# Kernel optimization log

Hardware: AMD Instinct MI355X
Metric: run time of the kernel (lower is better)

## Reference

```python
import jax, jax.numpy as jnp
import numpy as np

N = 50000          # number of keys
T = 12             # time_steps
Q = 3              # n_quantiles
H = 64             # hidden_channels
K = 32             # max children per key (keybom width)
NUM_LEVELS = 4     # hierarchy levels 0..3


def setup_inputs() -> dict:
    key = jax.random.key(0)
    k1, k2, k3, k4, k5, k6, k7 = jax.random.split(key, 7)
    gnn_embedding = jax.random.normal(k1, (N * T, H), dtype=jnp.float32)
    proj_w = jax.random.normal(k2, (H, Q), dtype=jnp.float32) * 0.1
    proj_b = jax.random.normal(k3, (Q,), dtype=jnp.float32) * 0.1
    # positive scaler (divided by later)
    scaler = jax.random.uniform(k4, (N, T), dtype=jnp.float32) + 0.5
    keybom = jax.random.randint(k5, (N, K), 0, N, dtype=jnp.int64)
    pad = jax.random.uniform(k6, (N, K)) < 0.3
    keybom = jnp.where(pad, jnp.int64(-1), keybom)
    key_level_index = jax.random.randint(k7, (N, 1), 0, NUM_LEVELS, dtype=jnp.int64)
    return {
        "gnn_embedding": gnn_embedding,
        "proj_w": proj_w,
        "proj_b": proj_b,
        "scaler": scaler,
        "keybom": keybom,
        "key_level_index": key_level_index,
        "num_levels": NUM_LEVELS,
    }


def reference(gnn_embedding, proj_w, proj_b, scaler, keybom, key_level_index, num_levels):
    n = scaler.shape[0]
    t = scaler.shape[1]
    q = proj_w.shape[1]
    # projection_layer + reshape (-1, time_steps, n_quantiles)
    out = (gnn_embedding @ proj_w + proj_b).reshape(n, t, q)  # [N,T,Q]
    # append dummy zero row (index n) used for -1 padding in keybom
    out = jnp.concatenate([out, jnp.zeros((1, t, q), out.dtype)], axis=0)      # [N+1,T,Q]
    sc = jnp.concatenate(
        [scaler[:, :, None], jnp.ones((1, t, 1), scaler.dtype)], axis=0
    )                                                                          # [N+1,T,1]
    kb = jnp.where(keybom < 0, n, keybom)  # -1 -> dummy row
    lvl = key_level_index[:, 0]
    # sequential hierarchical aggregation: level l reads level-(l-1)-updated out
    for level in range(1, num_levels):
        xw = out * sc                     # [N+1,T,Q]
        kl = xw[kb].sum(axis=1)           # gather [N,K,T,Q] -> sum over children
        new = kl / sc[:-1]                # rescale back
        mask = (lvl == level)[:, None, None]
        out = out.at[:-1].set(jnp.where(mask, new, out[:-1]))
    return out[:-1]
```

## Files before the change

### kernel.cpp

```cpp
#include <hip/hip_runtime.h>

#define NN 50000
#define TT 12
#define QQ 3
#define HH 64
#define KK 32
#define TQ 36
#define PW 9
#define NLEV 4

__device__ __forceinline__ float bf2f(unsigned int u16) {
    union { unsigned int i; float f; } c; c.i = u16 << 16; return c.f;
}
__device__ __forceinline__ unsigned short f2bf(float f) {
    union { float f; unsigned int i; } c; c.f = f;
    unsigned int u = c.i;
    u += 0x7FFFu + ((u >> 16) & 1u);
    return (unsigned short)(u >> 16);
}

__global__ __launch_bounds__(256) void proj_xw_kernel(
    const float* __restrict__ gnn, const float* __restrict__ w,
    const float* __restrict__ b, const float* __restrict__ scaler,
    unsigned short* __restrict__ xw, int nrows)
{
    const int lane = threadIdx.x & 63;
    const int sub  = lane & 15;
    const int h0   = sub * 4;

    float wreg[4][3];
#pragma unroll
    for (int j = 0; j < 4; ++j)
#pragma unroll
        for (int q = 0; q < 3; ++q)
            wreg[j][q] = w[(h0 + j) * 3 + q];
    const float b0 = b[0], b1 = b[1], b2 = b[2];

    const int gwave  = (blockIdx.x * blockDim.x + threadIdx.x) >> 6;
    const int nwaves = (gridDim.x * blockDim.x) >> 6;
    const int nquads = nrows >> 2;

    for (int quad = gwave; quad < nquads; quad += nwaves) {
        const float4 g = *reinterpret_cast<const float4*>(gnn + (size_t)quad * 256 + lane * 4);
        float a0 = g.x * wreg[0][0] + g.y * wreg[1][0] + g.z * wreg[2][0] + g.w * wreg[3][0];
        float a1 = g.x * wreg[0][1] + g.y * wreg[1][1] + g.z * wreg[2][1] + g.w * wreg[3][1];
        float a2 = g.x * wreg[0][2] + g.y * wreg[1][2] + g.z * wreg[2][2] + g.w * wreg[3][2];
#pragma unroll
        for (int off = 8; off > 0; off >>= 1) {
            a0 += __shfl_down(a0, off);
            a1 += __shfl_down(a1, off);
            a2 += __shfl_down(a2, off);
        }
        if (sub == 0) {
            const int row = quad * 4 + (lane >> 4);
            const float s = scaler[row];
            xw[row * 3 + 0] = f2bf((a0 + b0) * s);
            xw[row * 3 + 1] = f2bf((a1 + b1) * s);
            xw[row * 3 + 2] = f2bf((a2 + b2) * s);
        }
    }
}

__device__ __forceinline__ float4 gather_sum_quad(
    const uint2* __restrict__ cur64, const int* __restrict__ keybom,
    int node, int p)
{
    const int4* kb4 = reinterpret_cast<const int4*>(keybom + (size_t)node * KK);
    int keys[KK];
#pragma unroll
    for (int kk = 0; kk < KK / 4; ++kk) {
        const int4 k4 = kb4[kk];
        keys[kk * 4 + 0] = k4.x;
        keys[kk * 4 + 1] = k4.y;
        keys[kk * 4 + 2] = k4.z;
        keys[kk * 4 + 3] = k4.w;
    }
    uint2 u[KK];
#pragma unroll
    for (int k = 0; k < KK; ++k) {
        const int key = keys[k];
        u[k] = (key >= 0) ? cur64[(size_t)key * PW + p] : make_uint2(0u, 0u);
    }
    float a0 = 0.f, a1 = 0.f, a2 = 0.f, a3 = 0.f;
#pragma unroll
    for (int k = 0; k < KK; ++k) {
        a0 += bf2f(u[k].x & 0xFFFFu);
        a1 += bf2f(u[k].x >> 16);
        a2 += bf2f(u[k].y & 0xFFFFu);
        a3 += bf2f(u[k].y >> 16);
    }
    return make_float4(a0, a1, a2, a3);
}

__global__ __launch_bounds__(256) void level_kernel(
    const uint2* __restrict__ cur64, const int* __restrict__ keybom,
    const int* __restrict__ lvl, uint2* __restrict__ nxt64, int level)
{
    const int idx  = blockIdx.x * blockDim.x + threadIdx.x;
    if (idx >= NN * PW) return;
    const int node = idx / PW;
    const int p    = idx - node * PW;

    if (lvl[node] != level) {
        nxt64[idx] = cur64[idx];
        return;
    }
    const float4 s = gather_sum_quad(cur64, keybom, node, p);
    nxt64[idx] = make_uint2(
        (unsigned int)f2bf(s.x) | ((unsigned int)f2bf(s.y) << 16),
        (unsigned int)f2bf(s.z) | ((unsigned int)f2bf(s.w) << 16));
}

__global__ __launch_bounds__(256) void level_final_kernel(
    const uint2* __restrict__ cur64, const float* __restrict__ scaler,
    const int* __restrict__ keybom, const int* __restrict__ lvl,
    float* __restrict__ out, int level)
{
    const int idx  = blockIdx.x * blockDim.x + threadIdx.x;
    if (idx >= NN * PW) return;
    const int node = idx / PW;
    const int p    = idx - node * PW;

    float4 v;
    if (lvl[node] != level) {
        const uint2 u = cur64[idx];
        v = make_float4(bf2f(u.x & 0xFFFFu), bf2f(u.x >> 16),
                        bf2f(u.y & 0xFFFFu), bf2f(u.y >> 16));
    } else {
        v = gather_sum_quad(cur64, keybom, node, p);
    }
    const int e0 = node * TQ + 4 * p;
    const float4 r = make_float4(v.x / scaler[(e0 + 0) / 3],
                                 v.y / scaler[(e0 + 1) / 3],
                                 v.z / scaler[(e0 + 2) / 3],
                                 v.w / scaler[(e0 + 3) / 3]);
    *reinterpret_cast<float4*>(out + e0) = r;
}

extern "C" void kernel_launch(void* const* d_in, const int* in_sizes, int n_in,
                              void* d_out, int out_size, void* d_ws, size_t ws_size,
                              hipStream_t stream)
{
    const float* gnn    = (const float*)d_in[0];
    const float* w      = (const float*)d_in[1];
    const float* b      = (const float*)d_in[2];
    const float* scaler = (const float*)d_in[3];
    const int*   keybom = (const int*)d_in[4];
    const int*   lvl    = (const int*)d_in[5];
    float* out = (float*)d_out;

    char* ws = (char*)d_ws;
    unsigned short* bufA = (unsigned short*)ws;
    unsigned short* bufB = (unsigned short*)(ws + (size_t)NN * TQ * 2);

    proj_xw_kernel<<<2048, 256, 0, stream>>>(gnn, w, b, scaler, bufA, NN * TT);

    const int blocks = (NN * PW + 255) / 256;
    level_kernel<<<blocks, 256, 0, stream>>>((const uint2*)bufA, keybom, lvl,
                                             (uint2*)bufB, 1);
    level_kernel<<<blocks, 256, 0, stream>>>((const uint2*)bufB, keybom, lvl,
                                             (uint2*)bufA, 2);
    level_final_kernel<<<blocks, 256, 0, stream>>>((const uint2*)bufA, scaler,
                                                   keybom, lvl, out, 3);
}
```

Baseline: 64.18 us.

## Fuse three level kernels into one persistent kernel with grid barriers

Replaces the three per-level kernel launches with a single persistent kernel of 256 blocks of 512 threads. Grid-wide atomic spin barriers separate the phases, and the counters reset themselves for the next call. This removes two launch gaps and kernel tail effects. In exchange it relies on all 256 blocks being co-resident, which risks deadlock otherwise, and it lowers parallelism for the latency-bound gather phases.

```diff
diff --git a/kernel.cpp b/kernel.cpp
--- a/kernel.cpp
+++ b/kernel.cpp
@@ -9,6 +9,13 @@
 #define PW 9
 #define NLEV 4
 
+#define FB 256
+#define FT 512
+#define FN (FB * FT)
+#define ITEMS (NN * PW)
+
+__device__ unsigned g_bar0, g_bar1, g_fin;
+
 __device__ __forceinline__ float bf2f(unsigned int u16) {
     union { unsigned int i; float f; } c; c.i = u16 << 16; return c.f;
 }
@@ -70,10 +77,8 @@
 #pragma unroll
     for (int kk = 0; kk < KK / 4; ++kk) {
         const int4 k4 = kb4[kk];
-        keys[kk * 4 + 0] = k4.x;
-        keys[kk * 4 + 1] = k4.y;
-        keys[kk * 4 + 2] = k4.z;
-        keys[kk * 4 + 3] = k4.w;
+        keys[kk * 4 + 0] = k4.x; keys[kk * 4 + 1] = k4.y;
+        keys[kk * 4 + 2] = k4.z; keys[kk * 4 + 3] = k4.w;
     }
     uint2 u[KK];
 #pragma unroll
@@ -92,49 +97,90 @@
     return make_float4(a0, a1, a2, a3);
 }
 
-__global__ __launch_bounds__(256) void level_kernel(
-    const uint2* __restrict__ cur64, const int* __restrict__ keybom,
-    const int* __restrict__ lvl, uint2* __restrict__ nxt64, int level)
-{
-    const int idx  = blockIdx.x * blockDim.x + threadIdx.x;
-    if (idx >= NN * PW) return;
-    const int node = idx / PW;
-    const int p    = idx - node * PW;
-
-    if (lvl[node] != level) {
-        nxt64[idx] = cur64[idx];
-        return;
-    }
-    const float4 s = gather_sum_quad(cur64, keybom, node, p);
-    nxt64[idx] = make_uint2(
-        (unsigned int)f2bf(s.x) | ((unsigned int)f2bf(s.y) << 16),
-        (unsigned int)f2bf(s.z) | ((unsigned int)f2bf(s.w) << 16));
-}
-
-__global__ __launch_bounds__(256) void level_final_kernel(
-    const uint2* __restrict__ cur64, const float* __restrict__ scaler,
+__device__ __forceinline__ void gbar(unsigned* ctr, unsigned* prev)
+{
+    __syncthreads();
+    if (threadIdx.x == 0) {
+        const unsigned my = __hip_atomic_fetch_add(ctr, 1u, __ATOMIC_RELEASE,
+                                                   __HIP_MEMORY_SCOPE_AGENT);
+        if (prev != nullptr && my == FB - 1)
+            __hip_atomic_store(prev, 0u, __ATOMIC_RELAXED,
+                               __HIP_MEMORY_SCOPE_AGENT);
+        while (__hip_atomic_load(ctr, __ATOMIC_ACQUIRE,
+                                 __HIP_MEMORY_SCOPE_AGENT) < FB)
+            __builtin_amdgcn_s_sleep(1);
+    }
+    __syncthreads();
+}
+
+__device__ __forceinline__ void level_phase(
+    const uint2* __restrict__ src, uint2* __restrict__ dst,
     const int* __restrict__ keybom, const int* __restrict__ lvl,
-    float* __restrict__ out, int level)
-{
-    const int idx  = blockIdx.x * blockDim.x + threadIdx.x;
-    if (idx >= NN * PW) return;
-    const int node = idx / PW;
-    const int p    = idx - node * PW;
-
-    float4 v;
-    if (lvl[node] != level) {
-        const uint2 u = cur64[idx];
-        v = make_float4(bf2f(u.x & 0xFFFFu), bf2f(u.x >> 16),
-                        bf2f(u.y & 0xFFFFu), bf2f(u.y >> 16));
-    } else {
-        v = gather_sum_quad(cur64, keybom, node, p);
-    }
-    const int e0 = node * TQ + 4 * p;
-    const float4 r = make_float4(v.x / scaler[(e0 + 0) / 3],
-                                 v.y / scaler[(e0 + 1) / 3],
-                                 v.z / scaler[(e0 + 2) / 3],
-                                 v.w / scaler[(e0 + 3) / 3]);
-    *reinterpret_cast<float4*>(out + e0) = r;
+    int level, int gtid)
+{
+    for (int idx = gtid; idx < ITEMS; idx += FN) {
+        const int node = idx / PW;
+        const int p    = idx - node * PW;
+        if (lvl[node] != level) {
+            dst[idx] = src[idx];
+            continue;
+        }
+        const float4 s = gather_sum_quad(src, keybom, node, p);
+        dst[idx] = make_uint2(
+            (unsigned)f2bf(s.x) | ((unsigned)f2bf(s.y) << 16),
+            (unsigned)f2bf(s.z) | ((unsigned)f2bf(s.w) << 16));
+    }
+}
+
+__device__ __forceinline__ void final_phase(
+    const uint2* __restrict__ src, const float* __restrict__ scaler,
+    const int* __restrict__ keybom, const int* __restrict__ lvl,
+    float* __restrict__ out, int gtid)
+{
+    for (int idx = gtid; idx < ITEMS; idx += FN) {
+        const int node = idx / PW;
+        const int p    = idx - node * PW;
+        float4 v;
+        if (lvl[node] != 3) {
+            const uint2 u = src[idx];
+            v = make_float4(bf2f(u.x & 0xFFFFu), bf2f(u.x >> 16),
+                            bf2f(u.y & 0xFFFFu), bf2f(u.y >> 16));
+        } else {
+            v = gather_sum_quad(src, keybom, node, p);
+        }
+        const int e0 = node * TQ + 4 * p;
+        const float4 r = make_float4(v.x / scaler[(e0 + 0) / 3],
+                                     v.y / scaler[(e0 + 1) / 3],
+                                     v.z / scaler[(e0 + 2) / 3],
+                                     v.w / scaler[(e0 + 3) / 3]);
+        *reinterpret_cast<float4*>(out + e0) = r;
+    }
+}
+
+__global__ __launch_bounds__(FT) void fused_levels_kernel(
+    uint2* bufA, uint2* bufB, const float* __restrict__ scaler,
+    const int* __restrict__ keybom, const int* __restrict__ lvl,
+    float* __restrict__ out)
+{
+    const int gtid = blockIdx.x * FT + threadIdx.x;
+
+    level_phase(bufA, bufB, keybom, lvl, 1, gtid);
+    gbar(&g_bar0, nullptr);
+    level_phase(bufB, bufA, keybom, lvl, 2, gtid);
+    gbar(&g_bar1, &g_bar0);
+    final_phase(bufA, scaler, keybom, lvl, out, gtid);
+
+    __syncthreads();
+    if (threadIdx.x == 0) {
+        const unsigned my = __hip_atomic_fetch_add(&g_fin, 1u, __ATOMIC_RELEASE,
+                                                   __HIP_MEMORY_SCOPE_AGENT);
+        if (my == FB - 1) {
+            __hip_atomic_store(&g_bar1, 0u, __ATOMIC_RELAXED,
+                               __HIP_MEMORY_SCOPE_AGENT);
+            __hip_atomic_store(&g_fin, 0u, __ATOMIC_RELAXED,
+                               __HIP_MEMORY_SCOPE_AGENT);
+        }
+    }
 }
 
 extern "C" void kernel_launch(void* const* d_in, const int* in_sizes, int n_in,
@@ -154,12 +200,6 @@
     unsigned short* bufB = (unsigned short*)(ws + (size_t)NN * TQ * 2);
 
     proj_xw_kernel<<<2048, 256, 0, stream>>>(gnn, w, b, scaler, bufA, NN * TT);
-
-    const int blocks = (NN * PW + 255) / 256;
-    level_kernel<<<blocks, 256, 0, stream>>>((const uint2*)bufA, keybom, lvl,
-                                             (uint2*)bufB, 1);
-    level_kernel<<<blocks, 256, 0, stream>>>((const uint2*)bufB, keybom, lvl,
-                                             (uint2*)bufA, 2);
-    level_final_kernel<<<blocks, 256, 0, stream>>>((const uint2*)bufA, scaler,
-                                                   keybom, lvl, out, 3);
-}
+    fused_levels_kernel<<<FB, FT, 0, stream>>>((uint2*)bufA, (uint2*)bufB,
+                                               scaler, keybom, lvl, out);
+}
```

New measurement: 122.5 us. 1.91x slower.

## Encode child levels into keybom and drop per-level buffer copies

Applied to the files above, without the earlier changes.

Adds a prep kernel that packs each child's level tag into its keybom index. Level kernels then read the child's value from either the projected buffer P or an in-place final buffer F, chosen by level. Non-updated nodes are no longer copied between ping-pong buffers each level, which removes a full read and write pass per level. The cost is an extra prep pass over the whole keybom, and the encoding assumes keys fit in 16 bits.

```diff
diff --git a/kernel.cpp b/kernel.cpp
--- a/kernel.cpp
+++ b/kernel.cpp
@@ -17,6 +17,22 @@
     unsigned int u = c.i;
     u += 0x7FFFu + ((u >> 16) & 1u);
     return (unsigned short)(u >> 16);
+}
+
+__global__ __launch_bounds__(256) void prep_kernel(
+    const int* __restrict__ keybom, const int* __restrict__ lvl,
+    int* __restrict__ enc)
+{
+    const int idx = blockIdx.x * 256 + threadIdx.x;
+    if (idx >= NN * KK) return;
+    const int key = keybom[idx];
+    int e = -1;
+    if (key >= 0) {
+        int l = lvl[key];
+        l = (l == 0) ? 3 : l;
+        e = key | (l << 16);
+    }
+    enc[idx] = e;
 }
 
 __global__ __launch_bounds__(256) void proj_xw_kernel(
@@ -61,25 +77,25 @@
     }
 }
 
-__device__ __forceinline__ float4 gather_sum_quad(
-    const uint2* __restrict__ cur64, const int* __restrict__ keybom,
-    int node, int p)
+__device__ __forceinline__ float4 gather_FP(
+    const uint2* __restrict__ P2, const uint2* __restrict__ F2,
+    const int* __restrict__ enc, int node, int p, int level)
 {
-    const int4* kb4 = reinterpret_cast<const int4*>(keybom + (size_t)node * KK);
-    int keys[KK];
+    const int4* kb4 = reinterpret_cast<const int4*>(enc + (size_t)node * KK);
+    int e[KK];
 #pragma unroll
     for (int kk = 0; kk < KK / 4; ++kk) {
         const int4 k4 = kb4[kk];
-        keys[kk * 4 + 0] = k4.x;
-        keys[kk * 4 + 1] = k4.y;
-        keys[kk * 4 + 2] = k4.z;
-        keys[kk * 4 + 3] = k4.w;
+        e[kk * 4 + 0] = k4.x; e[kk * 4 + 1] = k4.y;
+        e[kk * 4 + 2] = k4.z; e[kk * 4 + 3] = k4.w;
     }
     uint2 u[KK];
 #pragma unroll
     for (int k = 0; k < KK; ++k) {
-        const int key = keys[k];
-        u[k] = (key >= 0) ? cur64[(size_t)key * PW + p] : make_uint2(0u, 0u);
+        const int ee  = e[k];
+        const int key = ee & 0xFFFF;
+        const uint2* src = (((ee >> 16) & 3) < level) ? F2 : P2;
+        u[k] = (ee >= 0) ? src[(size_t)key * PW + p] : make_uint2(0u, 0u);
     }
     float a0 = 0.f, a1 = 0.f, a2 = 0.f, a3 = 0.f;
 #pragma unroll
@@ -92,42 +108,40 @@
     return make_float4(a0, a1, a2, a3);
 }
 
-__global__ __launch_bounds__(256) void level_kernel(
-    const uint2* __restrict__ cur64, const int* __restrict__ keybom,
-    const int* __restrict__ lvl, uint2* __restrict__ nxt64, int level)
+__global__ __launch_bounds__(256) void levelF_kernel(
+    const uint2* __restrict__ P2, uint2* F2, const int* __restrict__ enc,
+    const int* __restrict__ lvl, int level)
 {
-    const int idx  = blockIdx.x * blockDim.x + threadIdx.x;
+    const int idx  = blockIdx.x * 256 + threadIdx.x;
+    if (idx >= NN * PW) return;
+    const int node = idx / PW;
+    if (lvl[node] != level) return;
+    const int p    = idx - node * PW;
+
+    const float4 s = gather_FP(P2, F2, enc, node, p, level);
+    F2[(size_t)node * PW + p] = make_uint2(
+        (unsigned)f2bf(s.x) | ((unsigned)f2bf(s.y) << 16),
+        (unsigned)f2bf(s.z) | ((unsigned)f2bf(s.w) << 16));
+}
+
+__global__ __launch_bounds__(256) void level3_final_kernel(
+    const uint2* __restrict__ P2, const uint2* __restrict__ F2,
+    const int* __restrict__ enc, const int* __restrict__ lvl,
+    const float* __restrict__ scaler, float* __restrict__ out)
+{
+    const int idx  = blockIdx.x * 256 + threadIdx.x;
     if (idx >= NN * PW) return;
     const int node = idx / PW;
     const int p    = idx - node * PW;
-
-    if (lvl[node] != level) {
-        nxt64[idx] = cur64[idx];
-        return;
-    }
-    const float4 s = gather_sum_quad(cur64, keybom, node, p);
-    nxt64[idx] = make_uint2(
-        (unsigned int)f2bf(s.x) | ((unsigned int)f2bf(s.y) << 16),
-        (unsigned int)f2bf(s.z) | ((unsigned int)f2bf(s.w) << 16));
-}
-
-__global__ __launch_bounds__(256) void level_final_kernel(
-    const uint2* __restrict__ cur64, const float* __restrict__ scaler,
-    const int* __restrict__ keybom, const int* __restrict__ lvl,
-    float* __restrict__ out, int level)
-{
-    const int idx  = blockIdx.x * blockDim.x + threadIdx.x;
-    if (idx >= NN * PW) return;
-    const int node = idx / PW;
-    const int p    = idx - node * PW;
+    const int l    = lvl[node];
 
     float4 v;
-    if (lvl[node] != level) {
-        const uint2 u = cur64[idx];
+    if (l == 3) {
+        v = gather_FP(P2, F2, enc, node, p, 3);
+    } else {
+        const uint2 u = ((l >= 1) ? F2 : P2)[(size_t)node * PW + p];
         v = make_float4(bf2f(u.x & 0xFFFFu), bf2f(u.x >> 16),
                         bf2f(u.y & 0xFFFFu), bf2f(u.y >> 16));
-    } else {
-        v = gather_sum_quad(cur64, keybom, node, p);
     }
     const int e0 = node * TQ + 4 * p;
     const float4 r = make_float4(v.x / scaler[(e0 + 0) / 3],
@@ -150,16 +164,17 @@
     float* out = (float*)d_out;
 
     char* ws = (char*)d_ws;
-    unsigned short* bufA = (unsigned short*)ws;
-    unsigned short* bufB = (unsigned short*)(ws + (size_t)NN * TQ * 2);
+    int*            encb = (int*)ws;
+    unsigned short* P    = (unsigned short*)(ws + (size_t)NN * KK * 4);
+    unsigned short* F    = (unsigned short*)(ws + (size_t)NN * KK * 4
+                                                + (size_t)NN * TQ * 2);
 
-    proj_xw_kernel<<<2048, 256, 0, stream>>>(gnn, w, b, scaler, bufA, NN * TT);
+    prep_kernel<<<(NN * KK + 255) / 256, 256, 0, stream>>>(keybom, lvl, encb);
+    proj_xw_kernel<<<2048, 256, 0, stream>>>(gnn, w, b, scaler, P, NN * TT);
 
     const int blocks = (NN * PW + 255) / 256;
-    level_kernel<<<blocks, 256, 0, stream>>>((const uint2*)bufA, keybom, lvl,
-                                             (uint2*)bufB, 1);
-    level_kernel<<<blocks, 256, 0, stream>>>((const uint2*)bufB, keybom, lvl,
-                                             (uint2*)bufA, 2);
-    level_final_kernel<<<blocks, 256, 0, stream>>>((const uint2*)bufA, scaler,
-                                                   keybom, lvl, out, 3);
+    levelF_kernel<<<blocks, 256, 0, stream>>>((const uint2*)P, (uint2*)F, encb, lvl, 1);
+    levelF_kernel<<<blocks, 256, 0, stream>>>((const uint2*)P, (uint2*)F, encb, lvl, 2);
+    level3_final_kernel<<<blocks, 256, 0, stream>>>((const uint2*)P, (const uint2*)F,
+                                                    encb, lvl, scaler, out);
 }
```

After: 73.73 us. +14.9%, slower.
